# Performance work log

Hardware: AMD Instinct MI355X
Metric: run time of the kernel (lower is better)

## Reference

```python
import jax, jax.numpy as jnp
import numpy as np
from jax import lax


def haar_dwt2(x):
    """Single-level 2D Haar (db1) DWT matching pywt sign conventions.
    x: (..., H, W) with H, W even. Returns (cA, cH, cV, cD) each (..., H/2, W/2).
    pywt db1: approx = (x0+x1)/sqrt2, detail = (x0-x1)/sqrt2; dwt2 keys:
    cH='da' (detail axis -2), cV='ad' (detail axis -1).
    """
    a = x[..., 0::2, 0::2]
    b = x[..., 0::2, 1::2]
    c = x[..., 1::2, 0::2]
    d = x[..., 1::2, 1::2]
    cA = (a + b + c + d) * 0.5
    cH = (a + b - c - d) * 0.5
    cV = (a - b + c - d) * 0.5
    cD = (a - b - c + d) * 0.5
    return cA, cH, cV, cD


def wavedec2_level2_array(x):
    """pywt.wavedec2(x, 'db1', level=2) followed by pywt.coeffs_to_array.
    x: (B, C, H, W) -> (B, C, H, W) coefficient array with layout:
      [[ [[cA2, cH2],[cV2, cD2]], cH1 ],
       [ cV1,                     cD1 ]]
    """
    cA1, cH1, cV1, cD1 = haar_dwt2(x)
    cA2, cH2, cV2, cD2 = haar_dwt2(cA1)
    lvl2 = jnp.concatenate([
        jnp.concatenate([cA2, cH2], axis=-1),
        jnp.concatenate([cV2, cD2], axis=-1),
    ], axis=-2)
    top = jnp.concatenate([lvl2, cH1], axis=-1)
    bot = jnp.concatenate([cV1, cD1], axis=-1)
    return jnp.concatenate([top, bot], axis=-2)


def setup_inputs() -> dict:
    key = jax.random.key(0)
    k1, k2, k3 = jax.random.split(key, 3)
    B, C, H = 128, 3, 224
    dim, patch = 768, 16
    x = jax.random.normal(k1, (B, C, H, H), dtype=jnp.float32)
    # Conv2d default init scale ~ 1/sqrt(fan_in)
    fan_in = C * patch * patch
    W = jax.random.normal(k2, (dim, C, patch, patch), dtype=jnp.float32) / np.sqrt(fan_in)
    b = jax.random.normal(k3, (dim,), dtype=jnp.float32) / np.sqrt(fan_in)
    return {"x": x, "W": W, "b": b}


def reference(x, W, b):
    patch = W.shape[-1]
    coeffs = wavedec2_level2_array(x)  # (B, C, H, W)
    y = lax.conv_general_dilated(
        coeffs, W,
        window_strides=(patch, patch),
        padding='VALID',
        dimension_numbers=('NCHW', 'OIHW', 'NCHW'),
    ) + b[None, :, None, None]          # (B, dim, H/p, W/p)
    B, D, Hp, Wp = y.shape
    return y.reshape(B, D, Hp * Wp).transpose(0, 2, 1)  # (B, seq, dim)
```

## Files before the change

kernel.cpp:

```cpp
#include <hip/hip_runtime.h>
#include <stdint.h>

typedef __attribute__((ext_vector_type(8))) __bf16 bf16x8;
typedef __attribute__((ext_vector_type(4))) float f32x4;

__device__ __forceinline__ unsigned short f2bf(float f) {
  union { float f; unsigned int u; } v; v.f = f;
  unsigned int u = v.u;
  return (unsigned short)((u + 0x7fffu + ((u >> 16) & 1u)) >> 16);
}

__device__ __forceinline__ void async_copy16(const void* g, void* s) {
  __builtin_amdgcn_global_load_lds(
      (__attribute__((address_space(1))) void*)const_cast<void*>(g),
      (__attribute__((address_space(3))) void*)s,
      16, 0, 0);
}

#define HAAR(a, bb, cc, dd, oA, oH, oV, oD)                                    \
  oA = 0.5f * ((a + bb) + (cc + dd));                                          \
  oH = 0.5f * ((a + bb) - (cc + dd));                                          \
  oV = 0.5f * ((a - bb) + (cc - dd));                                          \
  oD = 0.5f * ((a - bb) - (cc - dd));

__global__ __launch_bounds__(256) void convw_kernel(const float* __restrict__ W,
                                                    unsigned short* __restrict__ Wb) {
  int i = blockIdx.x * 256 + threadIdx.x;
  float4 v = ((const float4*)W)[i];
  uint2 o;
  o.x = (unsigned int)f2bf(v.x) | ((unsigned int)f2bf(v.y) << 16);
  o.y = (unsigned int)f2bf(v.z) | ((unsigned int)f2bf(v.w) << 16);
  ((uint2*)Wb)[i] = o;
}

__global__ __launch_bounds__(256) void dwt2_kernel(const float* __restrict__ x,
                                                   unsigned short* __restrict__ A) {
  int tid = blockIdx.x * 256 + threadIdx.x;
  int J = tid % 56;
  int t = tid / 56;
  int I = t % 56;
  t /= 56;
  int c = t % 3;
  int b = t / 3;

  const float* xp = x + (((size_t)t * 224 + 4 * I) * 224 + 4 * J);
  float4 r0 = *(const float4*)(xp);
  float4 r1 = *(const float4*)(xp + 224);
  float4 r2 = *(const float4*)(xp + 448);
  float4 r3 = *(const float4*)(xp + 672);

  float A1[2][2], H1[2][2], V1[2][2], D1[2][2];
  HAAR(r0.x, r0.y, r1.x, r1.y, A1[0][0], H1[0][0], V1[0][0], D1[0][0]);
  HAAR(r0.z, r0.w, r1.z, r1.w, A1[0][1], H1[0][1], V1[0][1], D1[0][1]);
  HAAR(r2.x, r2.y, r3.x, r3.y, A1[1][0], H1[1][0], V1[1][0], D1[1][0]);
  HAAR(r2.z, r2.w, r3.z, r3.w, A1[1][1], H1[1][1], V1[1][1], D1[1][1]);

  auto aidx = [&](int y, int xx) -> size_t {
    int mrow = b * 196 + (y >> 4) * 14 + (xx >> 4);
    int k = c * 256 + (y & 15) * 16 + (xx & 15);
    return (size_t)mrow * 768 + (size_t)k;
  };
  auto store2 = [&](int y, int xx, float v0, float v1) {
    unsigned int p = (unsigned int)f2bf(v0) | ((unsigned int)f2bf(v1) << 16);
    *(unsigned int*)(A + aidx(y, xx)) = p;
  };

  int y0 = 2 * I, x0 = 2 * J;
  store2(y0,           112 + x0, H1[0][0], H1[0][1]);
  store2(y0 + 1,       112 + x0, H1[1][0], H1[1][1]);
  store2(112 + y0,     x0,       V1[0][0], V1[0][1]);
  store2(112 + y0 + 1, x0,       V1[1][0], V1[1][1]);
  store2(112 + y0,     112 + x0, D1[0][0], D1[0][1]);
  store2(112 + y0 + 1, 112 + x0, D1[1][0], D1[1][1]);

  float vA2, vH2, vV2, vD2;
  HAAR(A1[0][0], A1[0][1], A1[1][0], A1[1][1], vA2, vH2, vV2, vD2);
  A[aidx(I,      J)]      = f2bf(vA2);
  A[aidx(I,      56 + J)] = f2bf(vH2);
  A[aidx(56 + I, J)]      = f2bf(vV2);
  A[aidx(56 + I, 56 + J)] = f2bf(vD2);
}

__global__ __launch_bounds__(256) void gemm_kernel(const unsigned short* __restrict__ A,
                                                   const unsigned short* __restrict__ Bt,
                                                   const float* __restrict__ bias,
                                                   float* __restrict__ C) {
  constexpr int K = 768, N = 768;
  constexpr int NT = 24;
  __shared__ unsigned short As[3][128 * 32];
  __shared__ unsigned short Bs[3][128 * 32];

  const int orig = blockIdx.x;
  const int tile = (orig & 7) * 147 + (orig >> 3);
  const int bm = tile / 6, bn = tile % 6;

  const int tid = threadIdx.x;
  const int lane = tid & 63;
  const int wave = tid >> 6;
  const int wr = wave >> 1, wc = wave & 1;
  const int mbase = bm * 128, nbase = bn * 128;

  f32x4 acc[4][4] = {};

  const int off0 = wave * 1024 + lane * 16;
  const int row0 = off0 >> 6;
  const int kc0 = (off0 >> 4) & 3;
  const int kcs = kc0 ^ ((row0 >> 1) & 3);
  const unsigned short* ga0 = A + (size_t)(mbase + row0) * K + kcs * 8;
  const unsigned short* ga1 = ga0 + (size_t)64 * K;
  const unsigned short* gb0 = Bt + (size_t)(nbase + row0) * K + kcs * 8;
  const unsigned short* gb1 = gb0 + (size_t)64 * K;

  auto stage = [&](int buf, int kt) {
    char* sa = (char*)As + buf * 8192 + wave * 1024;
    char* sb = (char*)Bs + buf * 8192 + wave * 1024;
    const int ko = kt * 32;
    async_copy16(ga0 + ko, sa);
    async_copy16(ga1 + ko, sa + 4096);
    async_copy16(gb0 + ko, sb);
    async_copy16(gb1 + ko, sb + 4096);
  };

  const int fr = lane & 15;
  const int kq = lane >> 4;
  const int chq = kq ^ ((fr >> 1) & 3);

  stage(0, 0);
  stage(1, 1);

#pragma unroll
  for (int kt = 0; kt < NT; ++kt) {
    if (kt < NT - 1)
      asm volatile("s_waitcnt vmcnt(4)" ::: "memory");
    else
      asm volatile("s_waitcnt vmcnt(0)" ::: "memory");
    __builtin_amdgcn_s_barrier();
    if (kt + 2 < NT) stage((kt + 2) % 3, kt + 2);

    const char* pa = (const char*)As + (kt % 3) * 8192 + (wr * 64 + fr) * 64 + chq * 16;
    const char* pb = (const char*)Bs + (kt % 3) * 8192 + (wc * 64 + fr) * 64 + chq * 16;
    bf16x8 af[4], bv[4];
#pragma unroll
    for (int mi = 0; mi < 4; ++mi) af[mi] = *(const bf16x8*)(pa + mi * 16 * 64);
#pragma unroll
    for (int ni = 0; ni < 4; ++ni) bv[ni] = *(const bf16x8*)(pb + ni * 16 * 64);
#pragma unroll
    for (int mi = 0; mi < 4; ++mi)
#pragma unroll
      for (int ni = 0; ni < 4; ++ni)
        acc[mi][ni] = __builtin_amdgcn_mfma_f32_16x16x32_bf16(af[mi], bv[ni],
                                                              acc[mi][ni], 0, 0, 0);
    asm volatile("s_waitcnt lgkmcnt(0)" ::: "memory");
  }

  const int rq = lane >> 4;
#pragma unroll
  for (int ni = 0; ni < 4; ++ni) {
    int n = nbase + wc * 64 + ni * 16 + fr;
    float bv = bias[n];
#pragma unroll
    for (int mi = 0; mi < 4; ++mi) {
      int mrow = mbase + wr * 64 + mi * 16 + rq * 4;
      f32x4 v = acc[mi][ni];
#pragma unroll
      for (int j = 0; j < 4; ++j) C[(size_t)(mrow + j) * N + n] = v[j] + bv;
    }
  }
}

extern "C" void kernel_launch(void* const* d_in, const int* in_sizes, int n_in,
                              void* d_out, int out_size, void* d_ws, size_t ws_size,
                              hipStream_t stream) {
  const float* x = (const float*)d_in[0];
  const float* W = (const float*)d_in[1];
  const float* bias = (const float*)d_in[2];
  float* out = (float*)d_out;

  unsigned short* A = (unsigned short*)d_ws;
  unsigned short* Wb = (unsigned short*)((char*)d_ws + 38535168);

  convw_kernel<<<576, 256, 0, stream>>>(W, Wb);
  dwt2_kernel<<<4704, 256, 0, stream>>>(x, A);
  gemm_kernel<<<1176, 256, 0, stream>>>(A, Wb, bias, out);
}
```

Before: 71.05 us.

## Deepen GEMM LDS pipeline to four stages and interleave loads with MFMA halves

Moves the GEMM mainloop from a 3-buffer to a 4-buffer LDS ring with three k-tiles in flight. Each iteration is split into two MFMA halves, with the A and B global-to-LDS copies issued separately between them and the fragment loads spread out. s_setprio raises wave priority around the MFMA bursts. The aim is to hide global load latency better and give a single barrier per iteration, at the cost of more LDS use (64KB), which may reduce occupancy.

```diff
diff --git a/kernel.cpp b/kernel.cpp
--- a/kernel.cpp
+++ b/kernel.cpp
@@ -87,8 +87,8 @@
                                                    float* __restrict__ C) {
   constexpr int K = 768, N = 768;
   constexpr int NT = 24;
-  __shared__ unsigned short As[3][128 * 32];
-  __shared__ unsigned short Bs[3][128 * 32];
+  __shared__ unsigned short As[4][128 * 32];
+  __shared__ unsigned short Bs[4][128 * 32];
 
   const int orig = blockIdx.x;
   const int tile = (orig & 7) * 147 + (orig >> 3);
@@ -111,46 +111,71 @@
   const unsigned short* gb0 = Bt + (size_t)(nbase + row0) * K + kcs * 8;
   const unsigned short* gb1 = gb0 + (size_t)64 * K;
 
-  auto stage = [&](int buf, int kt) {
+  auto stageA = [&](int buf, int kt) {
     char* sa = (char*)As + buf * 8192 + wave * 1024;
+    async_copy16(ga0 + kt * 32, sa);
+    async_copy16(ga1 + kt * 32, sa + 4096);
+  };
+  auto stageB = [&](int buf, int kt) {
     char* sb = (char*)Bs + buf * 8192 + wave * 1024;
-    const int ko = kt * 32;
-    async_copy16(ga0 + ko, sa);
-    async_copy16(ga1 + ko, sa + 4096);
-    async_copy16(gb0 + ko, sb);
-    async_copy16(gb1 + ko, sb + 4096);
+    async_copy16(gb0 + kt * 32, sb);
+    async_copy16(gb1 + kt * 32, sb + 4096);
   };
 
   const int fr = lane & 15;
   const int kq = lane >> 4;
   const int chq = kq ^ ((fr >> 1) & 3);
 
-  stage(0, 0);
-  stage(1, 1);
+  stageA(0, 0); stageB(0, 0);
+  stageA(1, 1); stageB(1, 1);
+  stageA(2, 2); stageB(2, 2);
+  asm volatile("s_waitcnt vmcnt(8)" ::: "memory");
+  __builtin_amdgcn_s_barrier();
 
 #pragma unroll
   for (int kt = 0; kt < NT; ++kt) {
-    if (kt < NT - 1)
-      asm volatile("s_waitcnt vmcnt(4)" ::: "memory");
-    else
-      asm volatile("s_waitcnt vmcnt(0)" ::: "memory");
-    __builtin_amdgcn_s_barrier();
-    if (kt + 2 < NT) stage((kt + 2) % 3, kt + 2);
-
-    const char* pa = (const char*)As + (kt % 3) * 8192 + (wr * 64 + fr) * 64 + chq * 16;
-    const char* pb = (const char*)Bs + (kt % 3) * 8192 + (wc * 64 + fr) * 64 + chq * 16;
+    const int cb = kt & 3;
+    const char* pa = (const char*)As + cb * 8192 + (wr * 64 + fr) * 64 + chq * 16;
+    const char* pb = (const char*)Bs + cb * 8192 + (wc * 64 + fr) * 64 + chq * 16;
     bf16x8 af[4], bv[4];
-#pragma unroll
-    for (int mi = 0; mi < 4; ++mi) af[mi] = *(const bf16x8*)(pa + mi * 16 * 64);
-#pragma unroll
-    for (int ni = 0; ni < 4; ++ni) bv[ni] = *(const bf16x8*)(pb + ni * 16 * 64);
-#pragma unroll
-    for (int mi = 0; mi < 4; ++mi)
+
+    if (kt + 3 < NT) stageA((kt + 3) & 3, kt + 3);
+#pragma unroll
+    for (int ni = 0; ni < 4; ++ni) bv[ni] = *(const bf16x8*)(pb + ni * 1024);
+    af[0] = *(const bf16x8*)(pa);
+    af[1] = *(const bf16x8*)(pa + 1024);
+    asm volatile("s_waitcnt lgkmcnt(0)" ::: "memory");
+    __builtin_amdgcn_sched_barrier(0);
+    __builtin_amdgcn_s_setprio(1);
+#pragma unroll
+    for (int mi = 0; mi < 2; ++mi)
 #pragma unroll
       for (int ni = 0; ni < 4; ++ni)
         acc[mi][ni] = __builtin_amdgcn_mfma_f32_16x16x32_bf16(af[mi], bv[ni],
                                                               acc[mi][ni], 0, 0, 0);
+    __builtin_amdgcn_s_setprio(0);
+
+    if (kt + 3 < NT) stageB((kt + 3) & 3, kt + 3);
+    af[2] = *(const bf16x8*)(pa + 2048);
+    af[3] = *(const bf16x8*)(pa + 3072);
     asm volatile("s_waitcnt lgkmcnt(0)" ::: "memory");
+    __builtin_amdgcn_sched_barrier(0);
+    __builtin_amdgcn_s_setprio(1);
+#pragma unroll
+    for (int mi = 2; mi < 4; ++mi)
+#pragma unroll
+      for (int ni = 0; ni < 4; ++ni)
+        acc[mi][ni] = __builtin_amdgcn_mfma_f32_16x16x32_bf16(af[mi], bv[ni],
+                                                              acc[mi][ni], 0, 0, 0);
+    __builtin_amdgcn_s_setprio(0);
+
+    if (kt <= NT - 4)
+      asm volatile("s_waitcnt vmcnt(8)" ::: "memory");
+    else if (kt == NT - 3)
+      asm volatile("s_waitcnt vmcnt(4)" ::: "memory");
+    else if (kt == NT - 2)
+      asm volatile("s_waitcnt vmcnt(0)" ::: "memory");
+    if (kt < NT - 1) __builtin_amdgcn_s_barrier();
   }
 
   const int rq = lane >> 4;
```

Measured after the change: 73.04 us. 2.8% more time.
